# Kernel tuning notes

Measured on AMD Instinct MI355X. Metric: run time of the kernel, lower is better.

## Reference

```python
import jax, jax.numpy as jnp
import numpy as np

B, T, H = 4, 2048, 1024
NH = 16
DK = H // NH  # 64
EPS = 1e-12


def setup_inputs() -> dict:
    key = jax.random.key(0)
    ks = jax.random.split(key, 20)
    s = 0.02
    inp = {
        "hidden_states": jax.random.normal(ks[0], (B, T, H), jnp.float32),
        "source_states": jax.random.normal(ks[1], (B, T, H), jnp.float32),
        "source_len": jax.random.randint(ks[2], (B,), 0, T, jnp.int64),
        # attention params (Linear: y = x @ W + b)
        "Wq": s * jax.random.normal(ks[3], (H, H), jnp.float32),
        "bq": jnp.zeros((H,), jnp.float32),
        "Wk": s * jax.random.normal(ks[4], (H, H), jnp.float32),
        "bk": jnp.zeros((H,), jnp.float32),
        "Wv": s * jax.random.normal(ks[5], (H, H), jnp.float32),
        "bv": jnp.zeros((H,), jnp.float32),
        "Wd": s * jax.random.normal(ks[6], (H, H), jnp.float32),
        "bd": jnp.zeros((H,), jnp.float32),
        # Fp: Linear -> ReLU -> (dropout, eval=id) -> Linear -> (dropout)
        "Wp1": s * jax.random.normal(ks[7], (H, H), jnp.float32),
        "bp1": jnp.zeros((H,), jnp.float32),
        "Wp2": s * jax.random.normal(ks[8], (H, H), jnp.float32),
        "bp2": jnp.zeros((H,), jnp.float32),
        # LayerNorm
        "ln_g": jnp.ones((H,), jnp.float32),
        "ln_b": jnp.zeros((H,), jnp.float32),
    }
    return inp


def _split_heads(x):
    # (B, T, H) -> (B, NH, T, DK)
    return x.reshape(B, T, NH, DK).transpose(0, 2, 1, 3)


def reference(hidden_states, source_states, source_len, Wq, bq, Wk, bk, Wv, bv,
              Wd, bd, Wp1, bp1, Wp2, bp2, ln_g, ln_b):
    # P = Fp(source_states), masked to valid source positions
    P = jax.nn.relu(source_states @ Wp1 + bp1) @ Wp2 + bp2  # (B,T,H)
    rng = jnp.arange(T)[None, :]                              # (1,T)
    source_mask = rng < source_len[:, None]                   # (B,T) bool
    P = P * source_mask[:, :, None].astype(P.dtype)

    q = _split_heads(hidden_states @ Wq + bq)  # (B,NH,T,DK)
    k = _split_heads(P @ Wk + bk)
    v = _split_heads(P @ Wv + bv)

    scores = jnp.einsum('bhqd,bhkd->bhqk', q, k) / jnp.sqrt(jnp.float32(DK))
    scores = scores + (1.0 - source_mask[:, None, None, :].astype(scores.dtype)) * -10000.0
    probs = jax.nn.softmax(scores.astype(jnp.float32), axis=-1).astype(hidden_states.dtype)

    ctx = jnp.einsum('bhqk,bhkd->bhqd', probs, v)            # (B,NH,T,DK)
    ctx = ctx.transpose(0, 2, 1, 3).reshape(B, T, H)

    attn_out = ctx @ Wd + bd
    x = attn_out + hidden_states
    mu = jnp.mean(x, axis=-1, keepdims=True)
    var = jnp.mean(jnp.square(x - mu), axis=-1, keepdims=True)
    out = (x - mu) * jax.lax.rsqrt(var + EPS) * ln_g + ln_b
    return out
```

## Files before the change

### kernel.cpp

```cpp
#include <hip/hip_runtime.h>
#include <hip/hip_bf16.h>

#define BB 4
#define TT 2048
#define HH 1024
#define NHH 16
#define DKK 64

typedef __attribute__((ext_vector_type(8))) short bf16x8;
typedef __attribute__((ext_vector_type(4))) float f32x4;

__device__ __forceinline__ unsigned short f2bf(float f) {
    union { float f; unsigned u; } v; v.f = f;
    unsigned r = v.u + 0x7fffu + ((v.u >> 16) & 1u);
    return (unsigned short)(r >> 16);
}

__device__ __forceinline__ void gload_lds16(const unsigned short* g, unsigned short* l) {
    __builtin_amdgcn_global_load_lds(
        (const __attribute__((address_space(1))) unsigned int*)g,
        (__attribute__((address_space(3))) unsigned int*)l, 16, 0, 0);
}

__global__ __launch_bounds__(256) void cvt2_kernel(const float* __restrict__ in0,
                                                   const float* __restrict__ in1,
                                                   unsigned short* __restrict__ out0,
                                                   unsigned short* __restrict__ out1, int n4) {
    const float* in = blockIdx.y ? in1 : in0;
    unsigned short* out = blockIdx.y ? out1 : out0;
    int i = blockIdx.x * blockDim.x + threadIdx.x;
    if (i < n4) {
        float4 v = reinterpret_cast<const float4*>(in)[i];
        union { unsigned short u[4]; unsigned long long ll; } o;
        o.u[0] = f2bf(v.x); o.u[1] = f2bf(v.y); o.u[2] = f2bf(v.z); o.u[3] = f2bf(v.w);
        reinterpret_cast<unsigned long long*>(out)[i] = o.ll;
    }
}

__global__ __launch_bounds__(256) void wtcvt6_kernel(
    const float* __restrict__ W0, const float* __restrict__ W1, const float* __restrict__ W2,
    const float* __restrict__ W3, const float* __restrict__ W4, const float* __restrict__ W5,
    unsigned short* __restrict__ T0, unsigned short* __restrict__ T1, unsigned short* __restrict__ T2,
    unsigned short* __restrict__ T3, unsigned short* __restrict__ T4, unsigned short* __restrict__ T5) {
    const float* W; unsigned short* Wt;
    switch (blockIdx.z) {
        case 0: W = W0; Wt = T0; break;
        case 1: W = W1; Wt = T1; break;
        case 2: W = W2; Wt = T2; break;
        case 3: W = W3; Wt = T3; break;
        case 4: W = W4; Wt = T4; break;
        default: W = W5; Wt = T5; break;
    }
    __shared__ float t[32][33];
    int bx = blockIdx.x * 32, by = blockIdx.y * 32;
    int tx = threadIdx.x, ty = threadIdx.y;
#pragma unroll
    for (int i = 0; i < 32; i += 8)
        t[ty + i][tx] = W[(size_t)(by + ty + i) * HH + bx + tx];
    __syncthreads();
#pragma unroll
    for (int i = 0; i < 32; i += 8)
        Wt[(size_t)(bx + ty + i) * HH + by + tx] = f2bf(t[tx][ty + i]);
}

template <int EPI, bool SKIP>
__global__ __launch_bounds__(256) void gemm_kernel(
    const unsigned short* __restrict__ A, const unsigned short* __restrict__ Bt,
    const float* __restrict__ bias, unsigned short* __restrict__ Cb,
    float* __restrict__ Cf, const float* __restrict__ resid,
    const int* __restrict__ slen, int M, int N, int K) {
    __shared__ unsigned short As[128 * 64];
    __shared__ unsigned short Bs[128 * 64];
    int flat = blockIdx.y * 8 + blockIdx.x;
    int xcd = flat & 7, idx = flat >> 3;
    int bx = (idx & 7) * 128;
    int by = (xcd + ((idx >> 3) << 3)) * 128;
    if constexpr (SKIP) {
        int slb = slen[by >> 11];
        int ktend = ((slb + 63) >> 6) << 6;
        if (ktend == 0) ktend = 64;
        if ((by & (TT - 1)) >= ktend) return;
    }
    int tid = threadIdx.x, lane = tid & 63, w = tid >> 6;
    int wr = (w >> 1) * 64, wc = (w & 1) * 64;

    f32x4 acc[4][4] = {};
    for (int k0 = 0; k0 < K; k0 += 64) {
        __syncthreads();
#pragma unroll
        for (int c = 0; c < 4; c++) {
            int idx2 = c * 256 + tid;
            int r = idx2 >> 3, col = (idx2 & 7) * 8;
            gload_lds16(&A[(size_t)(by + r) * K + k0 + col], &As[idx2 * 8]);
            gload_lds16(&Bt[(size_t)(bx + r) * K + k0 + col], &Bs[idx2 * 8]);
        }
        __syncthreads();
#pragma unroll
        for (int kk = 0; kk < 2; kk++) {
            bf16x8 a[4], b[4];
#pragma unroll
            for (int i = 0; i < 4; i++)
                a[i] = *(bf16x8*)&As[(wr + i * 16 + (lane & 15)) * 64 + kk * 32 + (lane >> 4) * 8];
#pragma unroll
            for (int j = 0; j < 4; j++)
                b[j] = *(bf16x8*)&Bs[(wc + j * 16 + (lane & 15)) * 64 + kk * 32 + (lane >> 4) * 8];
#pragma unroll
            for (int i = 0; i < 4; i++)
#pragma unroll
                for (int j = 0; j < 4; j++)
                    acc[i][j] = __builtin_amdgcn_mfma_f32_16x16x32_bf16(a[i], b[j], acc[i][j], 0, 0, 0);
        }
    }

    int sl = 0;
    if constexpr (EPI == 2) sl = slen[by >> 11];
#pragma unroll
    for (int i = 0; i < 4; i++)
#pragma unroll
        for (int j = 0; j < 4; j++)
#pragma unroll
            for (int r = 0; r < 4; r++) {
                int row = by + wr + i * 16 + (lane >> 4) * 4 + r;
                int col = bx + wc + j * 16 + (lane & 15);
                float v = acc[i][j][r] + bias[col];
                if constexpr (EPI == 1) v = fmaxf(v, 0.f);
                if constexpr (EPI == 2) { int t = row & (TT - 1); if (t >= sl) v = 0.f; }
                if constexpr (EPI == 6) v *= 0.18033688f;
                if constexpr (EPI == 1 || EPI == 2) {
                    Cb[(size_t)row * N + col] = f2bf(v);
                } else if constexpr (EPI == 3 || EPI == 6) {
                    int b = row >> 11, t = row & (TT - 1), h = col >> 6, d = col & 63;
                    Cb[((size_t)((b * NHH + h) * TT + t)) * DKK + d] = f2bf(v);
                } else if constexpr (EPI == 4) {
                    int b = row >> 11, t = row & (TT - 1), h = col >> 6, d = col & 63;
                    Cb[((size_t)((b * NHH + h) * DKK + d)) * TT + t] = f2bf(v);
                } else if constexpr (EPI == 5) {
                    Cf[(size_t)row * N + col] = v + resid[(size_t)row * N + col];
                }
            }
}

__global__ __launch_bounds__(512) void attn_kernel(
    const unsigned short* __restrict__ Q, const unsigned short* __restrict__ K,
    const unsigned short* __restrict__ Vt, const int* __restrict__ slen,
    unsigned short* __restrict__ ctx) {
    __shared__ unsigned short Ks[64 * 64];
    __shared__ unsigned short Vs[64 * 64];
    __shared__ unsigned short Pl[8][16 * 64];
    int tid = threadIdx.x, lane = tid & 63, w = tid >> 6;
    int c = lane & 15, g = lane >> 4;
    int flat = blockIdx.x;
    int bh = flat & 63;
    int q0 = (flat >> 6) * 128;
    int b = bh >> 4;
    size_t bhs = (size_t)bh;
    int sl = slen[b];
    int ktend = ((sl + 63) >> 6) << 6;
    if (ktend == 0) ktend = 64;

    bf16x8 qf[2];
    int qrow = q0 + w * 16 + c;
#pragma unroll
    for (int half = 0; half < 2; half++)
        qf[half] = *(const bf16x8*)&Q[(bhs * TT + qrow) * DKK + half * 32 + g * 8];

    char* Pw = (char*)&Pl[w][0];
    unsigned swz = (unsigned)((c & 7) << 4);

    int sr = tid >> 3, ss = tid & 7;
    int scol = (ss ^ (sr & 7)) * 8;

    float m_ = -INFINITY, l_ = 0.f;
    f32x4 o[4] = {};

    for (int kt = 0; kt < ktend; kt += 64) {
        __syncthreads();
        gload_lds16(&K[(bhs * TT + kt + sr) * DKK + scol], &Ks[tid * 8]);
        gload_lds16(&Vt[(bhs * DKK + sr) * TT + kt + scol], &Vs[tid * 8]);
        __syncthreads();

        f32x4 s[4] = {};
        __builtin_amdgcn_s_setprio(1);
#pragma unroll
        for (int j = 0; j < 4; j++)
#pragma unroll
            for (int half = 0; half < 2; half++) {
                bf16x8 kf = *(bf16x8*)((char*)Ks + (j * 16 + c) * 128 +
                                       (((unsigned)(half * 64 + g * 16)) ^ swz));
                s[j] = __builtin_amdgcn_mfma_f32_16x16x32_bf16(kf, qf[half], s[j], 0, 0, 0);
            }
        __builtin_amdgcn_s_setprio(0);

        if (kt + 64 > sl) {
#pragma unroll
            for (int j = 0; j < 4; j++) {
                int kbase = kt + j * 16 + g * 4;
#pragma unroll
                for (int r = 0; r < 4; r++)
                    if (kbase + r >= sl) s[j][r] = -14427.0f;
            }
        }

        float tmax = -INFINITY;
#pragma unroll
        for (int j = 0; j < 4; j++)
#pragma unroll
            for (int r = 0; r < 4; r++) tmax = fmaxf(tmax, s[j][r]);
        tmax = fmaxf(tmax, __shfl_xor(tmax, 16));
        tmax = fmaxf(tmax, __shfl_xor(tmax, 32));

        float p[4][4];
        float ps = 0.f;
        bool defer = __all(tmax <= m_ + 8.f);
        float mn = defer ? m_ : fmaxf(m_, tmax);
#pragma unroll
        for (int j = 0; j < 4; j++)
#pragma unroll
            for (int r = 0; r < 4; r++) {
                p[j][r] = __builtin_amdgcn_exp2f(s[j][r] - mn);
                ps += p[j][r];
            }
        ps += __shfl_xor(ps, 16);
        ps += __shfl_xor(ps, 32);
        if (defer) {
            l_ += ps;
        } else {
            float alpha = __builtin_amdgcn_exp2f(m_ - mn);
            l_ = l_ * alpha + ps;
            m_ = mn;
            float av[4];
#pragma unroll
            for (int r = 0; r < 4; r++) av[r] = __shfl(alpha, g * 4 + r);
#pragma unroll
            for (int go = 0; go < 4; go++)
#pragma unroll
                for (int r = 0; r < 4; r++) o[go][r] *= av[r];
        }

#pragma unroll
        for (int j = 0; j < 4; j++) {
            __hip_bfloat162 lo = __float22bfloat162_rn(make_float2(p[j][0], p[j][1]));
            __hip_bfloat162 hi = __float22bfloat162_rn(make_float2(p[j][2], p[j][3]));
            uint2 u;
            u.x = *(unsigned*)&lo;
            u.y = *(unsigned*)&hi;
            *(uint2*)(Pw + c * 128 + (((unsigned)(j * 32 + g * 8)) ^ swz)) = u;
        }
        bf16x8 pf0 = *(bf16x8*)(Pw + c * 128 + (((unsigned)(g * 16)) ^ swz));
        bf16x8 pf1 = *(bf16x8*)(Pw + c * 128 + (((unsigned)(64 + g * 16)) ^ swz));

        __builtin_amdgcn_s_setprio(1);
#pragma unroll
        for (int go = 0; go < 4; go++) {
            bf16x8 vf0 = *(bf16x8*)((char*)Vs + (go * 16 + c) * 128 +
                                    (((unsigned)(g * 16)) ^ swz));
            o[go] = __builtin_amdgcn_mfma_f32_16x16x32_bf16(pf0, vf0, o[go], 0, 0, 0);
            bf16x8 vf1 = *(bf16x8*)((char*)Vs + (go * 16 + c) * 128 +
                                    (((unsigned)(64 + g * 16)) ^ swz));
            o[go] = __builtin_amdgcn_mfma_f32_16x16x32_bf16(pf1, vf1, o[go], 0, 0, 0);
        }
        __builtin_amdgcn_s_setprio(0);
    }

    float linv[4];
#pragma unroll
    for (int r = 0; r < 4; r++) linv[r] = 1.f / __shfl(l_, g * 4 + r);
#pragma unroll
    for (int go = 0; go < 4; go++)
#pragma unroll
        for (int r = 0; r < 4; r++) {
            int t = q0 + w * 16 + g * 4 + r;
            int col = (bh & 15) * DKK + go * 16 + c;
            ctx[((size_t)(b * TT + t)) * HH + col] = f2bf(o[go][r] * linv[r]);
        }
}

__global__ __launch_bounds__(256) void ln_kernel(float* __restrict__ x,
                                                 const float* __restrict__ gam,
                                                 const float* __restrict__ bet) {
    int row = blockIdx.x, tid = threadIdx.x;
    float4 v = reinterpret_cast<float4*>(x)[(size_t)row * 256 + tid];
    float s = v.x + v.y + v.z + v.w;
#pragma unroll
    for (int m = 1; m < 64; m <<= 1) s += __shfl_xor(s, m);
    __shared__ float red[4], red2[4];
    if ((tid & 63) == 0) red[tid >> 6] = s;
    __syncthreads();
    float mean = (red[0] + red[1] + red[2] + red[3]) * (1.f / 1024.f);
    float dx0 = v.x - mean, dx1 = v.y - mean, dx2 = v.z - mean, dx3 = v.w - mean;
    float ss = dx0 * dx0 + dx1 * dx1 + dx2 * dx2 + dx3 * dx3;
#pragma unroll
    for (int m = 1; m < 64; m <<= 1) ss += __shfl_xor(ss, m);
    if ((tid & 63) == 0) red2[tid >> 6] = ss;
    __syncthreads();
    float var = (red2[0] + red2[1] + red2[2] + red2[3]) * (1.f / 1024.f);
    float rs = rsqrtf(var + 1e-12f);
    int c = tid * 4;
    float4 ov;
    ov.x = dx0 * rs * gam[c + 0] + bet[c + 0];
    ov.y = dx1 * rs * gam[c + 1] + bet[c + 1];
    ov.z = dx2 * rs * gam[c + 2] + bet[c + 2];
    ov.w = dx3 * rs * gam[c + 3] + bet[c + 3];
    reinterpret_cast<float4*>(x)[(size_t)row * 256 + tid] = ov;
}

extern "C" void kernel_launch(void* const* d_in, const int* in_sizes, int n_in,
                              void* d_out, int out_size, void* d_ws, size_t ws_size,
                              hipStream_t stream) {
    const float* hid  = (const float*)d_in[0];
    const float* src  = (const float*)d_in[1];
    const int* slen   = (const int*)d_in[2];
    const float* Wq  = (const float*)d_in[3];  const float* bq  = (const float*)d_in[4];
    const float* Wk  = (const float*)d_in[5];  const float* bk  = (const float*)d_in[6];
    const float* Wv  = (const float*)d_in[7];  const float* bv  = (const float*)d_in[8];
    const float* Wd  = (const float*)d_in[9];  const float* bd  = (const float*)d_in[10];
    const float* Wp1 = (const float*)d_in[11]; const float* bp1 = (const float*)d_in[12];
    const float* Wp2 = (const float*)d_in[13]; const float* bp2 = (const float*)d_in[14];
    const float* lng = (const float*)d_in[15]; const float* lnb = (const float*)d_in[16];

    char* ws = (char*)d_ws;
    const size_t MB = 1ull << 20;
    unsigned short* Wqt  = (unsigned short*)(ws + 0 * MB);
    unsigned short* Wkt  = (unsigned short*)(ws + 2 * MB);
    unsigned short* Wvt  = (unsigned short*)(ws + 4 * MB);
    unsigned short* Wdt  = (unsigned short*)(ws + 6 * MB);
    unsigned short* Wp1t = (unsigned short*)(ws + 8 * MB);
    unsigned short* Wp2t = (unsigned short*)(ws + 10 * MB);
    unsigned short* hidb = (unsigned short*)(ws + 12 * MB);
    unsigned short* srcb = (unsigned short*)(ws + 28 * MB);
    unsigned short* Ptmp = (unsigned short*)(ws + 44 * MB);
    unsigned short* Pb   = (unsigned short*)(ws + 60 * MB);
    unsigned short* Qb   = (unsigned short*)(ws + 76 * MB);
    unsigned short* Kb   = hidb;
    unsigned short* Vtb  = Ptmp;
    unsigned short* ctxb = srcb;

    wtcvt6_kernel<<<dim3(32, 32, 6), dim3(32, 8), 0, stream>>>(
        Wq, Wk, Wv, Wd, Wp1, Wp2, Wqt, Wkt, Wvt, Wdt, Wp1t, Wp2t);

    const int n4 = (BB * TT * HH) / 4;
    cvt2_kernel<<<dim3(n4 / 256, 2), 256, 0, stream>>>(hid, src, hidb, srcb, n4);

    dim3 gg(8, 64);
    gemm_kernel<1, true><<<gg, 256, 0, stream>>>(srcb, Wp1t, bp1, Ptmp, nullptr, nullptr, slen, BB * TT, HH, HH);
    gemm_kernel<2, true><<<gg, 256, 0, stream>>>(Ptmp, Wp2t, bp2, Pb, nullptr, nullptr, slen, BB * TT, HH, HH);
    gemm_kernel<6, false><<<gg, 256, 0, stream>>>(hidb, Wqt, bq, Qb, nullptr, nullptr, slen, BB * TT, HH, HH);
    gemm_kernel<3, true><<<gg, 256, 0, stream>>>(Pb, Wkt, bk, Kb, nullptr, nullptr, slen, BB * TT, HH, HH);
    gemm_kernel<4, true><<<gg, 256, 0, stream>>>(Pb, Wvt, bv, Vtb, nullptr, nullptr, slen, BB * TT, HH, HH);
    attn_kernel<<<dim3(64 * (TT / 128)), 512, 0, stream>>>(Qb, Kb, Vtb, slen, ctxb);
    gemm_kernel<5, false><<<gg, 256, 0, stream>>>(ctxb, Wdt, bd, nullptr, (float*)d_out, hid, slen, BB * TT, HH, HH);
    ln_kernel<<<BB * TT, 256, 0, stream>>>((float*)d_out, lng, lnb);
}
```

Measured before the change: 276.1 us.

## Fuse fp32-to-bf16 activation conversion into GEMM A-tile loads

Removes the separate conversion kernel for hidden and source states. The first projection GEMM and the Q GEMM now read fp32 activations directly and convert them to bf16 while staging the A tile into shared memory. This drops a full extra write and read of two bf16 activation tensors. In exchange, those GEMMs lose the async global-to-LDS path for A and load twice as many bytes per tile through registers. The attention grid is also relaid out from a flat index into a 3D (q-tile, head, batch) grid, which changes block scheduling order, and the workspace buffers are remapped.

```diff
diff --git a/kernel.cpp b/kernel.cpp
--- a/kernel.cpp
+++ b/kernel.cpp
@@ -16,25 +16,21 @@
     return (unsigned short)(r >> 16);
 }
 
+__device__ __forceinline__ bf16x8 cvt8(const float* __restrict__ p) {
+    float4 a = *(const float4*)p;
+    float4 b = *(const float4*)(p + 4);
+    bf16x8 r;
+    r[0] = (short)f2bf(a.x); r[1] = (short)f2bf(a.y);
+    r[2] = (short)f2bf(a.z); r[3] = (short)f2bf(a.w);
+    r[4] = (short)f2bf(b.x); r[5] = (short)f2bf(b.y);
+    r[6] = (short)f2bf(b.z); r[7] = (short)f2bf(b.w);
+    return r;
+}
+
 __device__ __forceinline__ void gload_lds16(const unsigned short* g, unsigned short* l) {
     __builtin_amdgcn_global_load_lds(
         (const __attribute__((address_space(1))) unsigned int*)g,
         (__attribute__((address_space(3))) unsigned int*)l, 16, 0, 0);
-}
-
-__global__ __launch_bounds__(256) void cvt2_kernel(const float* __restrict__ in0,
-                                                   const float* __restrict__ in1,
-                                                   unsigned short* __restrict__ out0,
-                                                   unsigned short* __restrict__ out1, int n4) {
-    const float* in = blockIdx.y ? in1 : in0;
-    unsigned short* out = blockIdx.y ? out1 : out0;
-    int i = blockIdx.x * blockDim.x + threadIdx.x;
-    if (i < n4) {
-        float4 v = reinterpret_cast<const float4*>(in)[i];
-        union { unsigned short u[4]; unsigned long long ll; } o;
-        o.u[0] = f2bf(v.x); o.u[1] = f2bf(v.y); o.u[2] = f2bf(v.z); o.u[3] = f2bf(v.w);
-        reinterpret_cast<unsigned long long*>(out)[i] = o.ll;
-    }
 }
 
 __global__ __launch_bounds__(256) void wtcvt6_kernel(
@@ -63,9 +59,10 @@
         Wt[(size_t)(bx + ty + i) * HH + by + tx] = f2bf(t[tx][ty + i]);
 }
 
-template <int EPI, bool SKIP>
+template <int EPI, bool SKIP, bool F32A>
 __global__ __launch_bounds__(256) void gemm_kernel(
-    const unsigned short* __restrict__ A, const unsigned short* __restrict__ Bt,
+    const unsigned short* __restrict__ A16, const float* __restrict__ A32,
+    const unsigned short* __restrict__ Bt,
     const float* __restrict__ bias, unsigned short* __restrict__ Cb,
     float* __restrict__ Cf, const float* __restrict__ resid,
     const int* __restrict__ slen, int M, int N, int K) {
@@ -91,7 +88,11 @@
         for (int c = 0; c < 4; c++) {
             int idx2 = c * 256 + tid;
             int r = idx2 >> 3, col = (idx2 & 7) * 8;
-            gload_lds16(&A[(size_t)(by + r) * K + k0 + col], &As[idx2 * 8]);
+            if constexpr (F32A) {
+                *(bf16x8*)&As[idx2 * 8] = cvt8(&A32[(size_t)(by + r) * K + k0 + col]);
+            } else {
+                gload_lds16(&A16[(size_t)(by + r) * K + k0 + col], &As[idx2 * 8]);
+            }
             gload_lds16(&Bt[(size_t)(bx + r) * K + k0 + col], &Bs[idx2 * 8]);
         }
         __syncthreads();
@@ -149,11 +150,8 @@
     __shared__ unsigned short Pl[8][16 * 64];
     int tid = threadIdx.x, lane = tid & 63, w = tid >> 6;
     int c = lane & 15, g = lane >> 4;
-    int flat = blockIdx.x;
-    int bh = flat & 63;
-    int q0 = (flat >> 6) * 128;
-    int b = bh >> 4;
-    size_t bhs = (size_t)bh;
+    int b = blockIdx.z, h = blockIdx.y, q0 = blockIdx.x * 128;
+    size_t bhs = (size_t)(b * NHH + h);
     int sl = slen[b];
     int ktend = ((sl + 63) >> 6) << 6;
     if (ktend == 0) ktend = 64;
@@ -270,7 +268,7 @@
 #pragma unroll
         for (int r = 0; r < 4; r++) {
             int t = q0 + w * 16 + g * 4 + r;
-            int col = (bh & 15) * DKK + go * 16 + c;
+            int col = h * DKK + go * 16 + c;
             ctx[((size_t)(b * TT + t)) * HH + col] = f2bf(o[go][r] * linv[r]);
         }
 }
@@ -326,28 +324,23 @@
     unsigned short* Wdt  = (unsigned short*)(ws + 6 * MB);
     unsigned short* Wp1t = (unsigned short*)(ws + 8 * MB);
     unsigned short* Wp2t = (unsigned short*)(ws + 10 * MB);
-    unsigned short* hidb = (unsigned short*)(ws + 12 * MB);
-    unsigned short* srcb = (unsigned short*)(ws + 28 * MB);
-    unsigned short* Ptmp = (unsigned short*)(ws + 44 * MB);
+    unsigned short* Kb   = (unsigned short*)(ws + 12 * MB);
+    unsigned short* ctxb = (unsigned short*)(ws + 28 * MB);
+    unsigned short* Vtb  = (unsigned short*)(ws + 44 * MB);
     unsigned short* Pb   = (unsigned short*)(ws + 60 * MB);
     unsigned short* Qb   = (unsigned short*)(ws + 76 * MB);
-    unsigned short* Kb   = hidb;
-    unsigned short* Vtb  = Ptmp;
-    unsigned short* ctxb = srcb;
+    unsigned short* Ptmp = ctxb;
 
     wtcvt6_kernel<<<dim3(32, 32, 6), dim3(32, 8), 0, stream>>>(
         Wq, Wk, Wv, Wd, Wp1, Wp2, Wqt, Wkt, Wvt, Wdt, Wp1t, Wp2t);
 
-    const int n4 = (BB * TT * HH) / 4;
-    cvt2_kernel<<<dim3(n4 / 256, 2), 256, 0, stream>>>(hid, src, hidb, srcb, n4);
-
     dim3 gg(8, 64);
-    gemm_kernel<1, true><<<gg, 256, 0, stream>>>(srcb, Wp1t, bp1, Ptmp, nullptr, nullptr, slen, BB * TT, HH, HH);
-    gemm_kernel<2, true><<<gg, 256, 0, stream>>>(Ptmp, Wp2t, bp2, Pb, nullptr, nullptr, slen, BB * TT, HH, HH);
-    gemm_kernel<6, false><<<gg, 256, 0, stream>>>(hidb, Wqt, bq, Qb, nullptr, nullptr, slen, BB * TT, HH, HH);
-    gemm_kernel<3, true><<<gg, 256, 0, stream>>>(Pb, Wkt, bk, Kb, nullptr, nullptr, slen, BB * TT, HH, HH);
-    gemm_kernel<4, true><<<gg, 256, 0, stream>>>(Pb, Wvt, bv, Vtb, nullptr, nullptr, slen, BB * TT, HH, HH);
-    attn_kernel<<<dim3(64 * (TT / 128)), 512, 0, stream>>>(Qb, Kb, Vtb, slen, ctxb);
-    gemm_kernel<5, false><<<gg, 256, 0, stream>>>(ctxb, Wdt, bd, nullptr, (float*)d_out, hid, slen, BB * TT, HH, HH);
+    gemm_kernel<1, true, true><<<gg, 256, 0, stream>>>(nullptr, src, Wp1t, bp1, Ptmp, nullptr, nullptr, slen, BB * TT, HH, HH);
+    gemm_kernel<2, true, false><<<gg, 256, 0, stream>>>(Ptmp, nullptr, Wp2t, bp2, Pb, nullptr, nullptr, slen, BB * TT, HH, HH);
+    gemm_kernel<6, false, true><<<gg, 256, 0, stream>>>(nullptr, hid, Wqt, bq, Qb, nullptr, nullptr, slen, BB * TT, HH, HH);
+    gemm_kernel<3, true, false><<<gg, 256, 0, stream>>>(Pb, nullptr, Wkt, bk, Kb, nullptr, nullptr, slen, BB * TT, HH, HH);
+    gemm_kernel<4, true, false><<<gg, 256, 0, stream>>>(Pb, nullptr, Wvt, bv, Vtb, nullptr, nullptr, slen, BB * TT, HH, HH);
+    attn_kernel<<<dim3(TT / 128, NHH, BB), 512, 0, stream>>>(Qb, Kb, Vtb, slen, ctxb);
+    gemm_kernel<5, false, false><<<gg, 256, 0, stream>>>(ctxb, nullptr, Wdt, bd, nullptr, (float*)d_out, hid, slen, BB * TT, HH, HH);
     ln_kernel<<<BB * TT, 256, 0, stream>>>((float*)d_out, lng, lnb);
 }
```

Measured after the change: 252.7 us. 1.09x faster.
